# Kernel tuning notes

Hardware: AMD Instinct MI355X
Metric: run time of the kernel (lower is better)

The kernel has to match this reference:

```python
import jax, jax.numpy as jnp
import numpy as np


def softsign(x):
    return x / (1.0 + jnp.abs(x))


def setup_inputs() -> dict:
    key = jax.random.key(0)
    ks = jax.random.split(key, 7)
    B = 1048576
    # Kaiming-ish small init to keep activations in softsign's linear-ish range
    x = jax.random.normal(ks[0], (B, 6), dtype=jnp.float32)
    W1 = jax.random.normal(ks[1], (6, 32), dtype=jnp.float32) * (1.0 / np.sqrt(6))
    b1 = jax.random.normal(ks[2], (32,), dtype=jnp.float32) * 0.01
    Wh = jax.random.normal(ks[3], (19, 32, 32), dtype=jnp.float32) * (1.0 / np.sqrt(32))
    bh = jax.random.normal(ks[4], (19, 32), dtype=jnp.float32) * 0.01
    Wout = jax.random.normal(ks[5], (32, 1), dtype=jnp.float32) * (1.0 / np.sqrt(32))
    bout = jax.random.normal(ks[6], (1,), dtype=jnp.float32) * 0.01
    return {"x": x, "W1": W1, "b1": b1, "Wh": Wh, "bh": bh, "Wout": Wout, "bout": bout}


def reference(x, W1, b1, Wh, bh, Wout, bout):
    # fc1 + softsign: [B,6] @ [6,32] -> [B,32]
    h = softsign(x @ W1 + b1)

    # 19 hidden Linear(32,32) + softsign layers, scanned over stacked weights
    def layer(h, wb):
        W, b = wb
        return softsign(h @ W + b), None

    h, _ = jax.lax.scan(layer, h, (Wh, bh))

    # fc6 (no activation): [B,32] @ [32,1] -> [B,1]
    return h @ Wout + bout
```

## Files before the change

### kernel.cpp

```cpp
#include <hip/hip_runtime.h>
#include <hip/hip_fp16.h>

typedef _Float16 f16x8 __attribute__((ext_vector_type(8)));
typedef float    f32x16 __attribute__((ext_vector_type(16)));

#define NLAYERS 19
#define BROWS   (1u << 20)
#define NTILES  (BROWS / 32)
#define NBLOCKS 512
#define TPB     1024
#define NWAVES  (NBLOCKS * (TPB / 64))


__device__ __forceinline__ int phi(int m) {
    return (m & ~12) | ((m & 4) << 1) | ((m & 8) >> 1);
}

__device__ __forceinline__ float fast_rcp(float a) {
    float r;
    asm("v_rcp_f32 %0, %1" : "=v"(r) : "v"(a));
    return r;
}

__device__ __forceinline__ unsigned pack_f16(float a, float b) {
    unsigned ra, rb;
    asm("v_cvt_f16_f32 %0, %1" : "=v"(ra) : "v"(a));
    asm("v_cvt_f16_f32 %0, %1" : "=v"(rb) : "v"(b));
    return __builtin_amdgcn_perm(rb, ra, 0x05040100u);
}

__device__ __forceinline__ f32x16 mfma_init_f16(f16x8 a, f16x8 b, const f32x16& cb) {
    f32x16 d;
    asm("v_mfma_f32_32x32x16_f16 %0, %1, %2, %3"
        : "=&v"(d) : "v"(a), "v"(b), "v"(cb));
    return d;
}
__device__ __forceinline__ void mfma_acc_f16(f16x8 a, f16x8 b, f32x16& c) {
    asm("v_mfma_f32_32x32x16_f16 %0, %1, %2, %0"
        : "+v"(c) : "v"(a), "v"(b));
}

union F16U { unsigned u[4]; f16x8 v; };

__device__ __forceinline__ void softsign16(const f32x16& c, float* sv) {
#pragma unroll
    for (int r = 0; r < 16; ++r) {
        float v = c[r];
        sv[r] = v * fast_rcp(1.0f + __builtin_fabsf(v));
    }
}

__device__ __forceinline__ void repack_f16(const float* sv, f16x8* hf) {
#pragma unroll
    for (int s = 0; s < 2; ++s) {
        F16U F;
#pragma unroll
        for (int j = 0; j < 4; ++j)
            F.u[j] = pack_f16(sv[8 * s + 2 * j], sv[8 * s + 2 * j + 1]);
        hf[s] = F.v;
    }
}

__device__ __forceinline__ void build_x_frag_f16(const float* xp, unsigned hm,
                                                 f16x8& bf) {
    const float2* xr = (const float2*)xp;
    float2 xa = xr[0], xb = xr[1], xc = xr[2];
    F16U B;
    B.u[0] = pack_f16(xa.x, xa.y) & hm;
    B.u[1] = pack_f16(xb.x, xb.y) & hm;
    B.u[2] = pack_f16(xc.x, xc.y) & hm;
    B.u[3] = 0u;
    bf = B.v;
}


extern "C" __global__ void __launch_bounds__(TPB, 4)
actuatornet_kernel(const float* __restrict__ x,  const float* __restrict__ W1,
                   const float* __restrict__ b1, const float* __restrict__ Wh,
                   const float* __restrict__ bh, const float* __restrict__ Wout,
                   const float* __restrict__ bout, float* __restrict__ out)
{
    __shared__ alignas(16) unsigned short s_wa_hi[NLAYERS * 2 * 64 * 8];
    __shared__ alignas(16) unsigned short s_wa_lo[NLAYERS * 2 * 64 * 8];
    __shared__ alignas(64) float s_bias[NLAYERS * 32];
    __shared__ alignas(64) float s_b1a[32];
    __shared__ alignas(64) float s_woa[32];

    const int tid = threadIdx.x;

    for (int idx = tid; idx < NLAYERS * 2 * 64 * 8; idx += TPB) {
        int e = idx & 7, l = (idx >> 3) & 63, s = (idx >> 9) & 1, lay = idx >> 10;
        int fi = 16 * s + 8 * (l >> 5) + e;
        int fo = phi(l & 31);
        float w = Wh[lay * 1024 + fi * 32 + fo];
        __half hw = __float2half(w);
        s_wa_hi[idx] = __half_as_ushort(hw);
        s_wa_lo[idx] = __half_as_ushort(__float2half(w - __half2float(hw)));
    }
    for (int idx = tid; idx < NLAYERS * 32; idx += TPB) {
        int r = idx & 15, h2 = (idx >> 4) & 1, lay = idx >> 5;
        int f = (r & 3) + 8 * (r >> 2) + 4 * h2;
        s_bias[idx] = bh[lay * 32 + phi(f)];
    }
    if (tid < 32) {
        int r = tid & 15, h2 = tid >> 4;
        int f = (r & 3) + 8 * (r >> 2) + 4 * h2;
        s_b1a[tid] = b1[phi(f)];
        s_woa[tid] = Wout[phi(f)];
    }
    const float bout_v = bout[0];

    const int lane = tid & 63;
    const int col  = lane & 31;
    const int h    = lane >> 5;
    const int wid  = blockIdx.x * (TPB / 64) + (tid >> 6);

    F16U A1H, A1L;
    {
        float w[8];
        const int fo1 = phi(col);
#pragma unroll
        for (int e = 0; e < 8; ++e) {
            int k = 8 * h + e;
            w[e] = (k < 6) ? W1[k * 32 + fo1] : 0.0f;
        }
#pragma unroll
        for (int j = 0; j < 4; ++j) {
            float a = w[2 * j], b = w[2 * j + 1];
            __half ha = __float2half(a), hb = __float2half(b);
            A1H.u[j] = (unsigned)__half_as_ushort(ha)
                     | ((unsigned)__half_as_ushort(hb) << 16);
            A1L.u[j] = (unsigned)__half_as_ushort(__float2half(a - __half2float(ha)))
                     | ((unsigned)__half_as_ushort(__float2half(b - __half2float(hb))) << 16);
        }
    }

    __syncthreads();

    const unsigned short* wa_hi_lane = s_wa_hi + lane * 8;
    const unsigned short* wa_lo_lane = s_wa_lo + lane * 8;
    const unsigned hm = (h == 0) ? 0xFFFFFFFFu : 0u;

    for (int tile = wid; tile < NTILES; tile += NWAVES) {
        const int base = tile * 32;

        f16x8 BF;
        build_x_frag_f16(x + (size_t)(base + col) * 6, hm, BF);

        const f32x16 cb1 = *(const f32x16*)(s_b1a + h * 16);
        f32x16 n = mfma_init_f16(A1H.v, BF, cb1);
        mfma_acc_f16(A1L.v, BF, n);

        float sv[16];
        f16x8 hf[2];
        softsign16(n, sv);
        repack_f16(sv, hf);

        for (int lay = 0; lay < NLAYERS; ++lay) {
            const f16x8 ah0 = *(const f16x8*)(wa_hi_lane + (lay * 2 + 0) * 512);
            const f16x8 ah1 = *(const f16x8*)(wa_hi_lane + (lay * 2 + 1) * 512);
            const f16x8 al0 = *(const f16x8*)(wa_lo_lane + (lay * 2 + 0) * 512);
            const f16x8 al1 = *(const f16x8*)(wa_lo_lane + (lay * 2 + 1) * 512);
            const f32x16 cb = *(const f32x16*)(s_bias + lay * 32 + h * 16);

            n = mfma_init_f16(ah0, hf[0], cb);
            mfma_acc_f16(ah1, hf[1], n);
            mfma_acc_f16(al0, hf[0], n);
            mfma_acc_f16(al1, hf[1], n);

            softsign16(n, sv);
            if (lay != NLAYERS - 1) repack_f16(sv, hf);
        }

        const f32x16 wo = *(const f32x16*)(s_woa + h * 16);
        float dot = 0.0f;
#pragma unroll
        for (int r = 0; r < 16; ++r) dot += sv[r] * wo[r];
        dot += __shfl_xor(dot, 32, 64);
        if (h == 0) out[base + col] = dot + bout_v;
    }
}


extern "C" void kernel_launch(void* const* d_in, const int* in_sizes, int n_in,
                              void* d_out, int out_size, void* d_ws, size_t ws_size,
                              hipStream_t stream) {
    const float* x    = (const float*)d_in[0];
    const float* W1   = (const float*)d_in[1];
    const float* b1   = (const float*)d_in[2];
    const float* Wh   = (const float*)d_in[3];
    const float* bh   = (const float*)d_in[4];
    const float* Wout = (const float*)d_in[5];
    const float* bout = (const float*)d_in[6];
    float* out = (float*)d_out;

    actuatornet_kernel<<<dim3(NBLOCKS), dim3(TPB), 0, stream>>>(
        x, W1, b1, Wh, bh, Wout, bout, out);
}
```

Measured before the change: 207.8 us.

## Process two independent 32-row tiles per wave to interleave MFMA chains

Each wave now handles a pair of 32-row tiles. It runs two independent MFMA accumulation chains per layer and shares the weight and bias LDS loads between them. The aim is to hide MFMA dependency latency and the softsign/repack VALU work of one tile behind the other's matrix ops. Softsign is also fused into the repack step. The cost is higher register pressure under launch_bounds(1024,4), with a risk of spills or lower occupancy.

```diff
diff --git a/kernel.cpp b/kernel.cpp
--- a/kernel.cpp
+++ b/kernel.cpp
@@ -6,7 +6,7 @@
 
 #define NLAYERS 19
 #define BROWS   (1u << 20)
-#define NTILES  (BROWS / 32)
+#define NPAIRS  (BROWS / 64)
 #define NBLOCKS 512
 #define TPB     1024
 #define NWAVES  (NBLOCKS * (TPB / 64))
@@ -50,13 +50,17 @@
     }
 }
 
-__device__ __forceinline__ void repack_f16(const float* sv, f16x8* hf) {
+__device__ __forceinline__ void act_repack(const f32x16& c, f16x8* hf) {
 #pragma unroll
     for (int s = 0; s < 2; ++s) {
         F16U F;
 #pragma unroll
-        for (int j = 0; j < 4; ++j)
-            F.u[j] = pack_f16(sv[8 * s + 2 * j], sv[8 * s + 2 * j + 1]);
+        for (int j = 0; j < 4; ++j) {
+            float a = c[8 * s + 2 * j], b = c[8 * s + 2 * j + 1];
+            float sa = a * fast_rcp(1.0f + __builtin_fabsf(a));
+            float sb = b * fast_rcp(1.0f + __builtin_fabsf(b));
+            F.u[j] = pack_f16(sa, sb);
+        }
         hf[s] = F.v;
     }
 }
@@ -141,20 +145,23 @@
     const unsigned short* wa_lo_lane = s_wa_lo + lane * 8;
     const unsigned hm = (h == 0) ? 0xFFFFFFFFu : 0u;
 
-    for (int tile = wid; tile < NTILES; tile += NWAVES) {
-        const int base = tile * 32;
-
-        f16x8 BF;
-        build_x_frag_f16(x + (size_t)(base + col) * 6, hm, BF);
+    for (int pair = wid; pair < NPAIRS; pair += NWAVES) {
+        const int baseA = pair * 64;
+        const int baseB = baseA + 32;
+
+        f16x8 BFa, BFb;
+        build_x_frag_f16(x + (size_t)(baseA + col) * 6, hm, BFa);
+        build_x_frag_f16(x + (size_t)(baseB + col) * 6, hm, BFb);
 
         const f32x16 cb1 = *(const f32x16*)(s_b1a + h * 16);
-        f32x16 n = mfma_init_f16(A1H.v, BF, cb1);
-        mfma_acc_f16(A1L.v, BF, n);
-
-        float sv[16];
-        f16x8 hf[2];
-        softsign16(n, sv);
-        repack_f16(sv, hf);
+        f32x16 nA = mfma_init_f16(A1H.v, BFa, cb1);
+        mfma_acc_f16(A1L.v, BFa, nA);
+        f32x16 nB = mfma_init_f16(A1H.v, BFb, cb1);
+        mfma_acc_f16(A1L.v, BFb, nB);
+
+        f16x8 hfA[2], hfB[2];
+        act_repack(nA, hfA);
+        act_repack(nB, hfB);
 
         for (int lay = 0; lay < NLAYERS; ++lay) {
             const f16x8 ah0 = *(const f16x8*)(wa_hi_lane + (lay * 2 + 0) * 512);
@@ -163,21 +170,36 @@
             const f16x8 al1 = *(const f16x8*)(wa_lo_lane + (lay * 2 + 1) * 512);
             const f32x16 cb = *(const f32x16*)(s_bias + lay * 32 + h * 16);
 
-            n = mfma_init_f16(ah0, hf[0], cb);
-            mfma_acc_f16(ah1, hf[1], n);
-            mfma_acc_f16(al0, hf[0], n);
-            mfma_acc_f16(al1, hf[1], n);
-
-            softsign16(n, sv);
-            if (lay != NLAYERS - 1) repack_f16(sv, hf);
-        }
+            nA = mfma_init_f16(ah0, hfA[0], cb);
+            mfma_acc_f16(ah1, hfA[1], nA);
+            mfma_acc_f16(al0, hfA[0], nA);
+            mfma_acc_f16(al1, hfA[1], nA);
+
+            nB = mfma_init_f16(ah0, hfB[0], cb);
+            mfma_acc_f16(ah1, hfB[1], nB);
+            mfma_acc_f16(al0, hfB[0], nB);
+            mfma_acc_f16(al1, hfB[1], nB);
+
+            if (lay != NLAYERS - 1) {
+                act_repack(nA, hfA);
+                act_repack(nB, hfB);
+            }
+        }
+
+        float svA[16], svB[16];
+        softsign16(nA, svA);
+        softsign16(nB, svB);
 
         const f32x16 wo = *(const f32x16*)(s_woa + h * 16);
-        float dot = 0.0f;
-#pragma unroll
-        for (int r = 0; r < 16; ++r) dot += sv[r] * wo[r];
-        dot += __shfl_xor(dot, 32, 64);
-        if (h == 0) out[base + col] = dot + bout_v;
+        float dA = 0.0f, dB = 0.0f;
+#pragma unroll
+        for (int r = 0; r < 16; ++r) { dA += svA[r] * wo[r]; dB += svB[r] * wo[r]; }
+        dA += __shfl_xor(dA, 32, 64);
+        dB += __shfl_xor(dB, 32, 64);
+        if (h == 0) {
+            out[baseA + col] = dA + bout_v;
+            out[baseB + col] = dB + bout_v;
+        }
     }
 }
 
```

Measured after the change: 197.4 us. -5.0%, faster.
